# Kernel optimization log

Measured on AMD Instinct MI355X. Metric: run time of the kernel, lower is better.

Reference implementation:

```python
import jax, jax.numpy as jnp
import numpy as np


def setup_inputs() -> dict:
    key = jax.random.key(0)
    k1, k2, k3, k4 = jax.random.split(key, 4)
    bs, ts0, tsk, f, nf = 32, 64, 64, 256, 128
    return {
        "x_0": jax.random.normal(k1, (bs, ts0, f), dtype=jnp.float32),
        "x_k": jax.random.normal(k2, (bs, tsk, f), dtype=jnp.float32),
        # Conv1d(1, nf, (ts0, tsk), stride=tsk) weight, in-channel dim of 1 dropped
        "conv_w": jax.random.normal(k3, (nf, ts0, tsk), dtype=jnp.float32) * 0.02,
        "conv_b": jax.random.normal(k4, (nf,), dtype=jnp.float32) * 0.02,
    }


def reference(x_0, x_k, conv_w, conv_b):
    # x_0: (bs, ts0, f), x_k: (bs, tsk, f)
    bs, ts0, f = x_0.shape
    tsk = x_k.shape[1]
    # Pairwise outer product over fields: (bs, f, ts0, tsk).
    z = jnp.einsum('btf,byf->bfty', x_0, x_k)
    # torch does .contiguous().view(bs, 1, ts0, f*tsk): a row-major flat
    # reinterpretation, identical to jnp.reshape; split the last axis back
    # into (f, tsk) to expose the stride-tsk conv windows.
    z = z.reshape(bs, ts0, f, tsk)
    # Conv kernel spans the full (ts0, tsk) window at each of the f output
    # positions (stride tsk) -> a weighted reduction per position + bias.
    out = jnp.einsum('btiy,nty->bni', z, conv_w) + conv_b[None, :, None]
    # matches .squeeze() of the torch (bs, nf, 1, f) conv output -> (bs, nf, f)
    return out
```

## Files before the change

### kernel.cpp

```cpp
#include <hip/hip_runtime.h>


__global__ __launch_bounds__(256)
void kg_kernel(const float* __restrict__ w, const float* __restrict__ xk,
               float* __restrict__ G) {
    __shared__ float Wl[64 * 64];
    __shared__ float Xl[64 * 64];

    const int tid = threadIdx.x;
    const int bid = blockIdx.x;
    const int t  = bid >> 2;
    const int nh = (bid >> 1) & 1;
    const int ch = bid & 1;

    #pragma unroll
    for (int r = 0; r < 4; ++r) {
        const int u  = tid + 256 * r;
        const int nl = u >> 4;
        const int yq = u & 15;
        const float4 v = *reinterpret_cast<const float4*>(
            w + (size_t)(nh * 64 + nl) * 4096 + t * 64 + 4 * yq);
        const int nu = nl >> 2, nd = nl & 3;
        const int y0 = 4 * yq;
        Wl[(y0 + 0) * 64 + ((nu ^ ((y0 + 0) & 15)) << 2) + nd] = v.x;
        Wl[(y0 + 1) * 64 + ((nu ^ ((y0 + 1) & 15)) << 2) + nd] = v.y;
        Wl[(y0 + 2) * 64 + ((nu ^ ((y0 + 2) & 15)) << 2) + nd] = v.z;
        Wl[(y0 + 3) * 64 + ((nu ^ ((y0 + 3) & 15)) << 2) + nd] = v.w;
    }
    #pragma unroll
    for (int r = 0; r < 4; ++r) {
        const int u  = tid + 256 * r;
        const int bb = u >> 6;
        const int y  = u & 63;
        const float4 v = *reinterpret_cast<const float4*>(
            xk + (size_t)(ch * 16 + bb) * 16384 + y * 256 + 4 * t);
        *reinterpret_cast<float4*>(&Xl[y * 64 + ((bb ^ (y & 15)) << 2)]) = v;
    }
    __syncthreads();

    const int cq = tid & 15;
    const int nq = tid >> 4;
    float acc[4][4] = {};
    #pragma unroll 8
    for (int y = 0; y < 64; ++y) {
        const int s = y & 15;
        const float4 wu = *reinterpret_cast<const float4*>(&Wl[y * 64 + ((nq ^ s) << 2)]);
        const float4 xu = *reinterpret_cast<const float4*>(&Xl[y * 64 + ((cq ^ s) << 2)]);
        acc[0][0] += wu.x * xu.x; acc[0][1] += wu.x * xu.y;
        acc[0][2] += wu.x * xu.z; acc[0][3] += wu.x * xu.w;
        acc[1][0] += wu.y * xu.x; acc[1][1] += wu.y * xu.y;
        acc[1][2] += wu.y * xu.z; acc[1][3] += wu.y * xu.w;
        acc[2][0] += wu.z * xu.x; acc[2][1] += wu.z * xu.y;
        acc[2][2] += wu.z * xu.z; acc[2][3] += wu.z * xu.w;
        acc[3][0] += wu.w * xu.x; acc[3][1] += wu.w * xu.y;
        acc[3][2] += wu.w * xu.z; acc[3][3] += wu.w * xu.w;
    }
    #pragma unroll
    for (int c = 0; c < 4; ++c) {
        const int col = ch * 64 + cq * 4 + c;
        const float4 v = make_float4(acc[0][c], acc[1][c], acc[2][c], acc[3][c]);
        *reinterpret_cast<float4*>(G + (size_t)(col * 64 + t) * 128 + nh * 64 + nq * 4) = v;
    }
}

__global__ __launch_bounds__(256)
void kout_kernel(const float* __restrict__ G, const float* __restrict__ x0,
                 const float* __restrict__ cb, float* __restrict__ out) {
    __shared__ float Gl[64 * 64];
    __shared__ float Xl[64 * 64];

    const int tid = threadIdx.x;
    const int bid = blockIdx.x;
    const int b   = bid >> 3;
    const int ihi = (bid >> 1) & 3;
    const int nh  = bid & 1;

    const size_t gbase = (size_t)(b * 4 + ihi) * 8192 + nh * 64;
    #pragma unroll
    for (int r = 0; r < 4; ++r) {
        const int u = tid + 256 * r;
        const int t = u >> 4;
        const int q = u & 15;
        const float4 v = *reinterpret_cast<const float4*>(G + gbase + (size_t)t * 128 + 4 * q);
        *reinterpret_cast<float4*>(&Gl[t * 64 + ((q ^ (t & 15)) << 2)]) = v;
    }
    #pragma unroll
    for (int r = 0; r < 16; ++r) {
        const int u  = tid + 256 * r;
        const int t  = u & 63;
        const int il = u >> 6;
        const float v = x0[(size_t)b * 16384 + il * 256 + 4 * t + ihi];
        Xl[t * 64 + (((il >> 2) ^ (t & 15)) << 2) + (il & 3)] = v;
    }
    __syncthreads();

    const int iu = tid & 15;
    const int nu = tid >> 4;
    float acc[4][4] = {};
    #pragma unroll 8
    for (int t = 0; t < 64; ++t) {
        const int s = t & 15;
        const float4 xv = *reinterpret_cast<const float4*>(&Xl[t * 64 + ((iu ^ s) << 2)]);
        const float4 gv = *reinterpret_cast<const float4*>(&Gl[t * 64 + ((nu ^ s) << 2)]);
        acc[0][0] += xv.x * gv.x; acc[0][1] += xv.x * gv.y;
        acc[0][2] += xv.x * gv.z; acc[0][3] += xv.x * gv.w;
        acc[1][0] += xv.y * gv.x; acc[1][1] += xv.y * gv.y;
        acc[1][2] += xv.y * gv.z; acc[1][3] += xv.y * gv.w;
        acc[2][0] += xv.z * gv.x; acc[2][1] += xv.z * gv.y;
        acc[2][2] += xv.z * gv.z; acc[2][3] += xv.z * gv.w;
        acc[3][0] += xv.w * gv.x; acc[3][1] += xv.w * gv.y;
        acc[3][2] += xv.w * gv.z; acc[3][3] += xv.w * gv.w;
    }
    const float4 cbv = *reinterpret_cast<const float4*>(cb + nh * 64 + nu * 4);
    #pragma unroll
    for (int g = 0; g < 4; ++g) {
        const int n = nh * 64 + nu * 4 + g;
        const float bias = (g == 0) ? cbv.x : (g == 1) ? cbv.y : (g == 2) ? cbv.z : cbv.w;
        const float4 v = make_float4(acc[0][g] + bias, acc[1][g] + bias,
                                     acc[2][g] + bias, acc[3][g] + bias);
        *reinterpret_cast<float4*>(out + (size_t)(b * 128 + n) * 256 + ihi * 64 + iu * 4) = v;
    }
}

extern "C" void kernel_launch(void* const* d_in, const int* in_sizes, int n_in,
                              void* d_out, int out_size, void* d_ws, size_t ws_size,
                              hipStream_t stream) {
    (void)in_sizes; (void)n_in; (void)out_size; (void)ws_size;
    const float* x0 = (const float*)d_in[0];
    const float* xk = (const float*)d_in[1];
    const float* w  = (const float*)d_in[2];
    const float* cb = (const float*)d_in[3];
    float* out = (float*)d_out;
    float* G   = (float*)d_ws;

    kg_kernel<<<dim3(256), dim3(256), 0, stream>>>(w, xk, G);
    kout_kernel<<<dim3(256), dim3(256), 0, stream>>>(G, x0, cb, out);
}
```

Before: 77.12 us.

## Replace FP32 FMA inner loops with split-bf16 MFMA in both GEMM kernels

```diff
diff --git a/kernel.cpp b/kernel.cpp
--- a/kernel.cpp
+++ b/kernel.cpp
@@ -1,12 +1,26 @@
 #include <hip/hip_runtime.h>
 
+
+typedef __attribute__((ext_vector_type(8))) short short8;
+typedef __attribute__((ext_vector_type(4))) float f32x4;
+
+__device__ __forceinline__ void split_bf16(float x, unsigned short& h, unsigned short& l) {
+    const unsigned int xb = __float_as_uint(x);
+    const unsigned int hb = xb & 0xFFFF0000u;
+    h = (unsigned short)(hb >> 16);
+    const float lo = x - __uint_as_float(hb);
+    const unsigned int lb = __float_as_uint(lo);
+    l = (unsigned short)((lb + 0x7FFFu + ((lb >> 16) & 1u)) >> 16);
+}
+
+__device__ __forceinline__ short8 frag_at(const unsigned short* arr, int row, int oct) {
+    return *reinterpret_cast<const short8*>(&arr[(row << 6) + (((oct ^ (row & 7)) << 3))]);
+}
 
 __global__ __launch_bounds__(256)
 void kg_kernel(const float* __restrict__ w, const float* __restrict__ xk,
                float* __restrict__ G) {
-    __shared__ float Wl[64 * 64];
-    __shared__ float Xl[64 * 64];
-
+    __shared__ unsigned short Ah[4096], Al[4096], Bh[4096], Bl[4096];
     const int tid = threadIdx.x;
     const int bid = blockIdx.x;
     const int t  = bid >> 2;
@@ -15,111 +29,142 @@
 
     #pragma unroll
     for (int r = 0; r < 4; ++r) {
-        const int u  = tid + 256 * r;
-        const int nl = u >> 4;
-        const int yq = u & 15;
-        const float4 v = *reinterpret_cast<const float4*>(
-            w + (size_t)(nh * 64 + nl) * 4096 + t * 64 + 4 * yq);
-        const int nu = nl >> 2, nd = nl & 3;
-        const int y0 = 4 * yq;
-        Wl[(y0 + 0) * 64 + ((nu ^ ((y0 + 0) & 15)) << 2) + nd] = v.x;
-        Wl[(y0 + 1) * 64 + ((nu ^ ((y0 + 1) & 15)) << 2) + nd] = v.y;
-        Wl[(y0 + 2) * 64 + ((nu ^ ((y0 + 2) & 15)) << 2) + nd] = v.z;
-        Wl[(y0 + 3) * 64 + ((nu ^ ((y0 + 3) & 15)) << 2) + nd] = v.w;
+        const int v  = tid + 256 * r;
+        const int n  = v >> 4;
+        const int yq = v & 15;
+        const float4 f = *reinterpret_cast<const float4*>(
+            w + (size_t)(nh * 64 + n) * 4096 + t * 64 + 4 * yq);
+        ushort4 ph, pl;
+        split_bf16(f.x, ph.x, pl.x); split_bf16(f.y, ph.y, pl.y);
+        split_bf16(f.z, ph.z, pl.z); split_bf16(f.w, ph.w, pl.w);
+        const int idx = (n << 6) + (((yq >> 1) ^ (n & 7)) << 3) + ((yq & 1) << 2);
+        *reinterpret_cast<ushort4*>(&Bh[idx]) = ph;
+        *reinterpret_cast<ushort4*>(&Bl[idx]) = pl;
     }
     #pragma unroll
     for (int r = 0; r < 4; ++r) {
-        const int u  = tid + 256 * r;
-        const int bb = u >> 6;
-        const int y  = u & 63;
-        const float4 v = *reinterpret_cast<const float4*>(
-            xk + (size_t)(ch * 16 + bb) * 16384 + y * 256 + 4 * t);
-        *reinterpret_cast<float4*>(&Xl[y * 64 + ((bb ^ (y & 15)) << 2)]) = v;
+        const int v  = tid + 256 * r;
+        const int bq = v >> 6;
+        const int y  = v & 63;
+        const float4 f = *reinterpret_cast<const float4*>(
+            xk + (size_t)(ch * 16 + bq) * 16384 + y * 256 + 4 * t);
+        const int o = y >> 3, yi = y & 7;
+        const float vals[4] = {f.x, f.y, f.z, f.w};
+        #pragma unroll
+        for (int jj = 0; jj < 4; ++jj) {
+            const int c = bq * 4 + jj;
+            unsigned short h, l;
+            split_bf16(vals[jj], h, l);
+            const int idx = (c << 6) + ((o ^ (c & 7)) << 3) + yi;
+            Ah[idx] = h; Al[idx] = l;
+        }
     }
     __syncthreads();
 
-    const int cq = tid & 15;
-    const int nq = tid >> 4;
-    float acc[4][4] = {};
-    #pragma unroll 8
-    for (int y = 0; y < 64; ++y) {
-        const int s = y & 15;
-        const float4 wu = *reinterpret_cast<const float4*>(&Wl[y * 64 + ((nq ^ s) << 2)]);
-        const float4 xu = *reinterpret_cast<const float4*>(&Xl[y * 64 + ((cq ^ s) << 2)]);
-        acc[0][0] += wu.x * xu.x; acc[0][1] += wu.x * xu.y;
-        acc[0][2] += wu.x * xu.z; acc[0][3] += wu.x * xu.w;
-        acc[1][0] += wu.y * xu.x; acc[1][1] += wu.y * xu.y;
-        acc[1][2] += wu.y * xu.z; acc[1][3] += wu.y * xu.w;
-        acc[2][0] += wu.z * xu.x; acc[2][1] += wu.z * xu.y;
-        acc[2][2] += wu.z * xu.z; acc[2][3] += wu.z * xu.w;
-        acc[3][0] += wu.w * xu.x; acc[3][1] += wu.w * xu.y;
-        acc[3][2] += wu.w * xu.z; acc[3][3] += wu.w * xu.w;
+    const int wv = tid >> 6, ln = tid & 63;
+    const int lr = ln & 15, lg = ln >> 4;
+    const int c0 = wv * 16;
+
+    f32x4 acc[4] = {{0.f,0.f,0.f,0.f},{0.f,0.f,0.f,0.f},{0.f,0.f,0.f,0.f},{0.f,0.f,0.f,0.f}};
+    #pragma unroll
+    for (int s = 0; s < 2; ++s) {
+        const int oct  = 4 * s + lg;
+        const int arow = c0 + lr;
+        const short8 a_h = frag_at(Ah, arow, oct);
+        const short8 a_l = frag_at(Al, arow, oct);
+        #pragma unroll
+        for (int nt = 0; nt < 4; ++nt) {
+            const int brow = nt * 16 + lr;
+            const short8 b_h = frag_at(Bh, brow, oct);
+            const short8 b_l = frag_at(Bl, brow, oct);
+            acc[nt] = __builtin_amdgcn_mfma_f32_16x16x32_bf16(a_h, b_h, acc[nt], 0, 0, 0);
+            acc[nt] = __builtin_amdgcn_mfma_f32_16x16x32_bf16(a_h, b_l, acc[nt], 0, 0, 0);
+            acc[nt] = __builtin_amdgcn_mfma_f32_16x16x32_bf16(a_l, b_h, acc[nt], 0, 0, 0);
+        }
     }
     #pragma unroll
-    for (int c = 0; c < 4; ++c) {
-        const int col = ch * 64 + cq * 4 + c;
-        const float4 v = make_float4(acc[0][c], acc[1][c], acc[2][c], acc[3][c]);
-        *reinterpret_cast<float4*>(G + (size_t)(col * 64 + t) * 128 + nh * 64 + nq * 4) = v;
-    }
+    for (int nt = 0; nt < 4; ++nt)
+        #pragma unroll
+        for (int r = 0; r < 4; ++r) {
+            const int c = ch * 64 + c0 + lg * 4 + r;
+            G[(size_t)c * 8192 + t * 128 + nh * 64 + nt * 16 + lr] = acc[nt][r];
+        }
 }
 
 __global__ __launch_bounds__(256)
 void kout_kernel(const float* __restrict__ G, const float* __restrict__ x0,
                  const float* __restrict__ cb, float* __restrict__ out) {
-    __shared__ float Gl[64 * 64];
-    __shared__ float Xl[64 * 64];
-
+    __shared__ unsigned short Ah[4096], Al[4096], Bh[4096], Bl[4096];
     const int tid = threadIdx.x;
     const int bid = blockIdx.x;
     const int b   = bid >> 3;
     const int ihi = (bid >> 1) & 3;
     const int nh  = bid & 1;
+    const int c   = b * 4 + ihi;
 
-    const size_t gbase = (size_t)(b * 4 + ihi) * 8192 + nh * 64;
     #pragma unroll
     for (int r = 0; r < 4; ++r) {
-        const int u = tid + 256 * r;
-        const int t = u >> 4;
-        const int q = u & 15;
-        const float4 v = *reinterpret_cast<const float4*>(G + gbase + (size_t)t * 128 + 4 * q);
-        *reinterpret_cast<float4*>(&Gl[t * 64 + ((q ^ (t & 15)) << 2)]) = v;
+        const int v  = tid + 256 * r;
+        const int tt = v >> 4;
+        const int nq = v & 15;
+        const float4 f = *reinterpret_cast<const float4*>(
+            G + (size_t)c * 8192 + tt * 128 + nh * 64 + 4 * nq);
+        const int o = tt >> 3, ti = tt & 7;
+        const float vals[4] = {f.x, f.y, f.z, f.w};
+        #pragma unroll
+        for (int q = 0; q < 4; ++q) {
+            const int n = 4 * nq + q;
+            unsigned short h, l;
+            split_bf16(vals[q], h, l);
+            const int idx = (n << 6) + ((o ^ (n & 7)) << 3) + ti;
+            Ah[idx] = h; Al[idx] = l;
+        }
     }
     #pragma unroll
     for (int r = 0; r < 16; ++r) {
-        const int u  = tid + 256 * r;
-        const int t  = u & 63;
-        const int il = u >> 6;
-        const float v = x0[(size_t)b * 16384 + il * 256 + 4 * t + ihi];
-        Xl[t * 64 + (((il >> 2) ^ (t & 15)) << 2) + (il & 3)] = v;
+        const int v  = tid + 256 * r;
+        const int il = v >> 6;
+        const int tt = v & 63;
+        const float x = x0[(size_t)b * 16384 + il * 256 + 4 * tt + ihi];
+        unsigned short h, l;
+        split_bf16(x, h, l);
+        const int idx = (il << 6) + (((tt >> 3) ^ (il & 7)) << 3) + (tt & 7);
+        Bh[idx] = h; Bl[idx] = l;
     }
     __syncthreads();
 
-    const int iu = tid & 15;
-    const int nu = tid >> 4;
-    float acc[4][4] = {};
-    #pragma unroll 8
-    for (int t = 0; t < 64; ++t) {
-        const int s = t & 15;
-        const float4 xv = *reinterpret_cast<const float4*>(&Xl[t * 64 + ((iu ^ s) << 2)]);
-        const float4 gv = *reinterpret_cast<const float4*>(&Gl[t * 64 + ((nu ^ s) << 2)]);
-        acc[0][0] += xv.x * gv.x; acc[0][1] += xv.x * gv.y;
-        acc[0][2] += xv.x * gv.z; acc[0][3] += xv.x * gv.w;
-        acc[1][0] += xv.y * gv.x; acc[1][1] += xv.y * gv.y;
-        acc[1][2] += xv.y * gv.z; acc[1][3] += xv.y * gv.w;
-        acc[2][0] += xv.z * gv.x; acc[2][1] += xv.z * gv.y;
-        acc[2][2] += xv.z * gv.z; acc[2][3] += xv.z * gv.w;
-        acc[3][0] += xv.w * gv.x; acc[3][1] += xv.w * gv.y;
-        acc[3][2] += xv.w * gv.z; acc[3][3] += xv.w * gv.w;
+    const int wv = tid >> 6, ln = tid & 63;
+    const int lr = ln & 15, lg = ln >> 4;
+    const int n0 = wv * 16;
+
+    f32x4 acc[4] = {{0.f,0.f,0.f,0.f},{0.f,0.f,0.f,0.f},{0.f,0.f,0.f,0.f},{0.f,0.f,0.f,0.f}};
+    #pragma unroll
+    for (int s = 0; s < 2; ++s) {
+        const int oct  = 4 * s + lg;
+        const int arow = n0 + lr;
+        const short8 a_h = frag_at(Ah, arow, oct);
+        const short8 a_l = frag_at(Al, arow, oct);
+        #pragma unroll
+        for (int it = 0; it < 4; ++it) {
+            const int brow = it * 16 + lr;
+            const short8 b_h = frag_at(Bh, brow, oct);
+            const short8 b_l = frag_at(Bl, brow, oct);
+            acc[it] = __builtin_amdgcn_mfma_f32_16x16x32_bf16(a_h, b_h, acc[it], 0, 0, 0);
+            acc[it] = __builtin_amdgcn_mfma_f32_16x16x32_bf16(a_h, b_l, acc[it], 0, 0, 0);
+            acc[it] = __builtin_amdgcn_mfma_f32_16x16x32_bf16(a_l, b_h, acc[it], 0, 0, 0);
+        }
     }
-    const float4 cbv = *reinterpret_cast<const float4*>(cb + nh * 64 + nu * 4);
+    float bias[4];
     #pragma unroll
-    for (int g = 0; g < 4; ++g) {
-        const int n = nh * 64 + nu * 4 + g;
-        const float bias = (g == 0) ? cbv.x : (g == 1) ? cbv.y : (g == 2) ? cbv.z : cbv.w;
-        const float4 v = make_float4(acc[0][g] + bias, acc[1][g] + bias,
-                                     acc[2][g] + bias, acc[3][g] + bias);
-        *reinterpret_cast<float4*>(out + (size_t)(b * 128 + n) * 256 + ihi * 64 + iu * 4) = v;
-    }
+    for (int r = 0; r < 4; ++r) bias[r] = cb[nh * 64 + n0 + lg * 4 + r];
+    #pragma unroll
+    for (int it = 0; it < 4; ++it)
+        #pragma unroll
+        for (int r = 0; r < 4; ++r) {
+            const int n = nh * 64 + n0 + lg * 4 + r;
+            out[(size_t)b * 32768 + (size_t)n * 256 + ihi * 64 + it * 16 + lr]
+                = acc[it][r] + bias[r];
+        }
 }
 
 extern "C" void kernel_launch(void* const* d_in, const int* in_sizes, int n_in,
```

Measured after the change: 71.38 us. -7.4%, faster.
